# Kernel optimization log

Measured on AMD Instinct MI355X. Metric: run time of the kernel, lower is better.

## Reference

```python
import jax, jax.numpy as jnp
import numpy as np

B, N, D = 4, 2048, 1024
HEAD_DIMS = 128
NUM_HEADS = 8
PROJ = HEAD_DIMS * NUM_HEADS  # 1024


def setup_inputs() -> dict:
    key = jax.random.key(0)
    ks = jax.random.split(key, 5)
    # Weights stored as (in, out); xavier-normal-like scale
    def xavier(k, fan_in, fan_out):
        std = (2.0 / (fan_in + fan_out)) ** 0.5
        return jax.random.normal(k, (fan_in, fan_out), dtype=jnp.float32) * std
    return {
        "x": jax.random.normal(ks[0], (B, N, D), dtype=jnp.float32),
        "Wq": xavier(ks[1], D, PROJ),
        "Wk": xavier(ks[2], D, PROJ),
        "Wv": xavier(ks[3], D, PROJ),
        "Wo": xavier(ks[4], PROJ, PROJ),
    }


def reference(x, Wq, Wk, Wv, Wo):
    b, n, d = x.shape
    # QKV projections, split into heads: (b, h, n, hd)
    def split_heads(z):
        return z.reshape(b, n, NUM_HEADS, HEAD_DIMS).transpose(0, 2, 1, 3)
    q = split_heads(x @ Wq)
    k = split_heads(x @ Wk)
    v = split_heads(x @ Wv)
    scale = 1.0 / jnp.sqrt(jnp.float32(HEAD_DIMS))
    logits = jnp.einsum("bhqd,bhkd->bhqk", q, k) * scale
    weights = jax.nn.softmax(logits, axis=-1)
    out = jnp.einsum("bhqk,bhkd->bhqd", weights, v)
    out = out.transpose(0, 2, 1, 3).reshape(b, n, PROJ)
    return out @ Wo
```

## Files before the change

### kernel.cpp

```cpp
#include <hip/hip_runtime.h>
#include <hip/hip_bf16.h>


typedef __attribute__((ext_vector_type(8))) short short8;
typedef __attribute__((ext_vector_type(4))) short short4v;
typedef __attribute__((ext_vector_type(4))) float floatx4;

#define MFMA_BF16(a, b, c) __builtin_amdgcn_mfma_f32_16x16x32_bf16((a), (b), (c), 0, 0, 0)

static constexpr int BATCH  = 4;
static constexpr int NHEADS = 8;
static constexpr int SEQ    = 2048;
static constexpr int HD     = 128;
static constexpr int DMODEL = 1024;
static constexpr int MROWS  = BATCH * SEQ;
static constexpr int NQKV   = 3 * DMODEL;

static __device__ __forceinline__ short bf16bits(float v) {
    __hip_bfloat16 h = __float2bfloat16(v);
    return *reinterpret_cast<short*>(&h);
}

template <typename T>
static __device__ __forceinline__ short8 load8_bf16(const T* p) {
    if constexpr (sizeof(T) == 2) {
        return *(const short8*)p;
    } else {
        const float4 f0 = *(const float4*)p;
        const float4 f1 = *(const float4*)(p + 4);
        short8 r;
        r[0] = bf16bits(f0.x); r[1] = bf16bits(f0.y);
        r[2] = bf16bits(f0.z); r[3] = bf16bits(f0.w);
        r[4] = bf16bits(f1.x); r[5] = bf16bits(f1.y);
        r[6] = bf16bits(f1.z); r[7] = bf16bits(f1.w);
        return r;
    }
}

static __device__ __forceinline__ void storeC(float* C, size_t idx, float v) {
    C[idx] = v;
}
static __device__ __forceinline__ void storeC(__hip_bfloat16* C, size_t idx, float v) {
    C[idx] = __float2bfloat16(v);
}

static __device__ __forceinline__ void gload16(const short* g, short* l) {
    __builtin_amdgcn_global_load_lds(
        (const __attribute__((address_space(1))) void*)g,
        (__attribute__((address_space(3))) void*)l, 16, 0, 0);
}

__global__ __launch_bounds__(256)
void convert_bf16(const float* __restrict__ in, short* __restrict__ out)
{
    const size_t i = ((size_t)blockIdx.x * 256 + threadIdx.x) * 8;
    *(short8*)&out[i] = load8_bf16(&in[i]);
}

__global__ __launch_bounds__(256)
void transpose_w(const float* __restrict__ W, short* __restrict__ Wt, int K, int N)
{
    __shared__ short T[32][33];
    const int n0 = blockIdx.x * 32, k0 = blockIdx.y * 32;
    const int r = threadIdx.x >> 3, c4 = (threadIdx.x & 7) * 4;

    const float4 v = *(const float4*)&W[(size_t)(k0 + r) * N + n0 + c4];
    T[r][c4 + 0] = bf16bits(v.x);
    T[r][c4 + 1] = bf16bits(v.y);
    T[r][c4 + 2] = bf16bits(v.z);
    T[r][c4 + 3] = bf16bits(v.w);
    __syncthreads();

    short4v o;
    o[0] = T[c4 + 0][r]; o[1] = T[c4 + 1][r];
    o[2] = T[c4 + 2][r]; o[3] = T[c4 + 3][r];
    *(short4v*)&Wt[(size_t)(n0 + r) * K + k0 + c4] = o;
}

template <typename OutT, bool QKV>
__global__ __launch_bounds__(256)
void gemm128(const short* __restrict__ A, const short* __restrict__ Bt,
             OutT* __restrict__ C, int M, int N, int K)
{
    __shared__ __align__(16) short As[128 * 32];
    __shared__ __align__(16) short Bs[128 * 32];

    const int tid  = threadIdx.x;
    const int lane = tid & 63;
    const int w    = tid >> 6;
    const int quad = lane >> 4;
    const int l16  = lane & 15;

    const int m0 = blockIdx.x * 128;
    const int n0 = blockIdx.y * 128;
    const int wm = (w >> 1) * 64;
    const int wn = (w & 1) * 64;

    floatx4 acc[4][4] = {};

    const int srow = w * 32 + (lane >> 2);
    const int sk   = (lane & 3) ^ ((srow >> 1) & 3);
    const short* aG = A  + (size_t)(m0 + srow) * K + sk * 8;
    const short* bG = Bt + (size_t)(n0 + srow) * K + sk * 8;
    short* aL = As + w * 1024 + lane * 8;
    short* bL = Bs + w * 1024 + lane * 8;

    const int fsw = (l16 >> 1) & 3;

    for (int k0 = 0; k0 < K; k0 += 32) {
        __syncthreads();
        gload16(aG + k0,                   aL);
        gload16(aG + k0 + (size_t)16 * K,  aL + 512);
        gload16(bG + k0,                   bL);
        gload16(bG + k0 + (size_t)16 * K,  bL + 512);
        __syncthreads();

        short8 af[4], bf[4];
        #pragma unroll
        for (int mi = 0; mi < 4; ++mi)
            af[mi] = *(short8*)&As[(wm + mi * 16 + l16) * 32 + (quad ^ fsw) * 8];
        #pragma unroll
        for (int ni = 0; ni < 4; ++ni)
            bf[ni] = *(short8*)&Bs[(wn + ni * 16 + l16) * 32 + (quad ^ fsw) * 8];

        #pragma unroll
        for (int mi = 0; mi < 4; ++mi)
            #pragma unroll
            for (int ni = 0; ni < 4; ++ni)
                acc[mi][ni] = MFMA_BF16(af[mi], bf[ni], acc[mi][ni]);
    }

    const size_t bufElems = (size_t)MROWS * DMODEL;
    #pragma unroll
    for (int mi = 0; mi < 4; ++mi)
        #pragma unroll
        for (int ni = 0; ni < 4; ++ni)
            #pragma unroll
            for (int r = 0; r < 4; ++r) {
                const int m = m0 + wm + mi * 16 + quad * 4 + r;
                const int n = n0 + wn + ni * 16 + l16;
                const float v = acc[mi][ni][r];
                if constexpr (QKV) {
                    const int qkv = n >> 10, rem = n & 1023;
                    const int h = rem >> 7, d = rem & 127;
                    const int b = m >> 11, s = m & 2047;
                    if (qkv == 2)
                        storeC(C, 2 * bufElems +
                                  (((size_t)b * NHEADS + h) * HD + d) * SEQ + s, v);
                    else
                        storeC(C, qkv * bufElems +
                                  (((size_t)b * NHEADS + h) * SEQ + s) * HD + d, v);
                } else {
                    storeC(C, (size_t)m * N + n, v);
                }
            }
}

__global__ __launch_bounds__(256)
void attn_flash2(const short* __restrict__ Q, const short* __restrict__ K,
                 const short* __restrict__ Vt, __hip_bfloat16* __restrict__ O)
{
    __shared__ __align__(16) short Ks[32 * 128];
    __shared__ __align__(16) short Vs[128 * 32];
    __shared__ __align__(16) short Plds[4][16 * 40];

    const int tid  = threadIdx.x;
    const int lane = tid & 63;
    const int w    = tid >> 6;
    const int quad = lane >> 4;
    const int l16  = lane & 15;

    const int q0 = blockIdx.x * 64;
    const int h  = blockIdx.y;
    const int b  = blockIdx.z;

    const short* Qh  = Q  + (((size_t)b * NHEADS + h) * SEQ) * HD;
    const short* Kh  = K  + (((size_t)b * NHEADS + h) * SEQ) * HD;
    const short* Vth = Vt + (((size_t)b * NHEADS + h) * HD) * SEQ;

    const float scale = 0.08838834764831845f;

    const int qrow = q0 + w * 16 + l16;
    short8 qf[4];
    #pragma unroll
    for (int c = 0; c < 4; ++c)
        qf[c] = *(const short8*)&Qh[(size_t)qrow * HD + c * 32 + quad * 8];

    const int krow0 = w * 8 + (lane >> 4);
    const int kp    = lane & 15;
    const short* kG0 = Kh + (size_t)krow0 * HD + (kp ^ (krow0 & 15)) * 8;
    const short* kG1 = Kh + (size_t)(krow0 + 4) * HD + (kp ^ ((krow0 + 4) & 15)) * 8;
    short* kL0 = Ks + w * 1024 + lane * 8;
    short* kL1 = kL0 + 512;
    const int vrow0 = w * 32 + (lane >> 2);
    const int vp    = lane & 3;
    const short* vG0 = Vth + (size_t)vrow0 * SEQ + (vp ^ ((vrow0 >> 1) & 3)) * 8;
    const short* vG1 = vG0 + (size_t)16 * SEQ;
    short* vL0 = Vs + w * 1024 + lane * 8;
    short* vL1 = vL0 + 512;

    float lrow[4] = {0.f, 0.f, 0.f, 0.f};
    floatx4 acc[8] = {};

    const int fswK = l16;
    const int fswV = (l16 >> 1) & 3;
    short* Pw = &Plds[w][0];

    for (int kt = 0; kt < SEQ; kt += 32) {
        __syncthreads();
        gload16(kG0, kL0);
        gload16(kG1, kL1);
        gload16(vG0, vL0);
        gload16(vG1, vL1);
        kG0 += 32 * HD; kG1 += 32 * HD;
        vG0 += 32;      vG1 += 32;
        __syncthreads();

        floatx4 s0 = {}, s1 = {};
        #pragma unroll
        for (int c = 0; c < 4; ++c) {
            const int k_ = c * 4 + quad;
            short8 kf0 = *(short8*)&Ks[l16 * 128 + (k_ ^ fswK) * 8];
            short8 kf1 = *(short8*)&Ks[(16 + l16) * 128 + (k_ ^ fswK) * 8];
            s0 = MFMA_BF16(qf[c], kf0, s0);
            s1 = MFMA_BF16(qf[c], kf1, s1);
        }

        float p0[4], p1[4];
        #pragma unroll
        for (int r = 0; r < 4; ++r) {
            p0[r] = __expf(fminf(s0[r] * scale, 20.f));
            p1[r] = __expf(fminf(s1[r] * scale, 20.f));
            lrow[r] += p0[r] + p1[r];
        }

        #pragma unroll
        for (int r = 0; r < 4; ++r) {
            Pw[(quad * 4 + r) * 40 + l16]      = bf16bits(p0[r]);
            Pw[(quad * 4 + r) * 40 + 16 + l16] = bf16bits(p1[r]);
        }
        short8 pf = *(short8*)&Pw[l16 * 40 + quad * 8];

        #pragma unroll
        for (int hc = 0; hc < 8; ++hc) {
            short8 vf = *(short8*)&Vs[(hc * 16 + l16) * 32 + (quad ^ fswV) * 8];
            acc[hc] = MFMA_BF16(pf, vf, acc[hc]);
        }
    }

    #pragma unroll
    for (int r = 0; r < 4; ++r) {
        lrow[r] += __shfl_xor(lrow[r], 1);
        lrow[r] += __shfl_xor(lrow[r], 2);
        lrow[r] += __shfl_xor(lrow[r], 4);
        lrow[r] += __shfl_xor(lrow[r], 8);
    }

    #pragma unroll
    for (int hc = 0; hc < 8; ++hc)
        #pragma unroll
        for (int r = 0; r < 4; ++r) {
            const int row = q0 + w * 16 + quad * 4 + r;
            const float val = acc[hc][r] / fmaxf(lrow[r], 1e-30f);
            O[((size_t)b * SEQ + row) * DMODEL + h * HD + hc * 16 + l16] =
                __float2bfloat16(val);
        }
}

template <typename AT, typename OutT>
__global__ __launch_bounds__(256)
void gemm64(const AT* __restrict__ A, const float* __restrict__ W,
            OutT* __restrict__ C, int M, int N, int K, int headsplit)
{
    __shared__ __align__(16) short As[64][32];
    __shared__ __align__(16) short Bs[64][32];

    const int tid  = threadIdx.x;
    const int lane = tid & 63;
    const int w    = tid >> 6;
    const int quad = lane >> 4;
    const int l16  = lane & 15;

    const int m0 = blockIdx.x * 64;
    const int n0 = blockIdx.y * 64;
    const int wm = (w >> 1) * 32;
    const int wn = (w & 1) * 32;

    floatx4 acc[2][2] = {};

    const int arow = tid >> 2, acol = (tid & 3) * 8;
    const int brow = tid >> 3, bcol = (tid & 7) * 8;

    const AT*    aptr = A + (size_t)(m0 + arow) * K + acol;
    const float* bptr = W + (size_t)brow * N + n0 + bcol;

    for (int k0 = 0; k0 < K; k0 += 32) {
        short8 av = load8_bf16(aptr + k0);
        short8 bv = load8_bf16(bptr + (size_t)k0 * N);
        __syncthreads();
        *(short8*)&As[arow][acol] = av;
        #pragma unroll
        for (int j = 0; j < 8; ++j)
            Bs[bcol + j][brow] = bv[j];
        __syncthreads();

        short8 af0 = *(short8*)&As[wm + l16][quad * 8];
        short8 af1 = *(short8*)&As[wm + 16 + l16][quad * 8];
        short8 bf0 = *(short8*)&Bs[wn + l16][quad * 8];
        short8 bf1 = *(short8*)&Bs[wn + 16 + l16][quad * 8];

        acc[0][0] = MFMA_BF16(af0, bf0, acc[0][0]);
        acc[0][1] = MFMA_BF16(af0, bf1, acc[0][1]);
        acc[1][0] = MFMA_BF16(af1, bf0, acc[1][0]);
        acc[1][1] = MFMA_BF16(af1, bf1, acc[1][1]);
    }

    #pragma unroll
    for (int mi = 0; mi < 2; ++mi)
        #pragma unroll
        for (int ni = 0; ni < 2; ++ni)
            #pragma unroll
            for (int r = 0; r < 4; ++r) {
                const int m = m0 + wm + mi * 16 + quad * 4 + r;
                const int n = n0 + wn + ni * 16 + l16;
                const float v = acc[mi][ni][r];
                if (headsplit) {
                    const int b = m >> 11, nn = m & 2047;
                    const int h = n >> 7,  d  = n & 127;
                    storeC(C, (((size_t)b * NHEADS + h) * SEQ + nn) * HD + d, v);
                } else {
                    storeC(C, (size_t)m * N + n, v);
                }
            }
}

__global__ __launch_bounds__(256)
void attn_flash(const short* __restrict__ Q, const short* __restrict__ K,
                const short* __restrict__ V, __hip_bfloat16* __restrict__ O)
{
    __shared__ __align__(16) short Ks[32][136];
    __shared__ __align__(16) short Vtl[HD][40];
    __shared__ __align__(16) short Plds[4][16][40];

    const int tid  = threadIdx.x;
    const int lane = tid & 63;
    const int w    = tid >> 6;
    const int quad = lane >> 4;
    const int l16  = lane & 15;

    const int q0 = blockIdx.x * 64;
    const int h  = blockIdx.y;
    const int b  = blockIdx.z;

    const size_t headoff = ((size_t)b * NHEADS + h) * SEQ * HD;
    const short* Qh = Q + headoff;
    const short* Kh = K + headoff;
    const short* Vh = V + headoff;

    const float scale = 0.08838834764831845f;

    const int qrow = q0 + w * 16 + l16;
    short8 qf[4];
    #pragma unroll
    for (int c = 0; c < 4; ++c)
        qf[c] = *(const short8*)&Qh[(size_t)qrow * HD + c * 32 + quad * 8];

    float mrow[4], lrow[4];
    #pragma unroll
    for (int r = 0; r < 4; ++r) { mrow[r] = -1e30f; lrow[r] = 0.f; }
    floatx4 acc[8] = {};

    const int krow = tid >> 4, kcol = (tid & 15) * 8;
    const int vkey = tid & 31;
    const int vhd  = (tid >> 5) * 16;

    for (int kt = 0; kt < SEQ; kt += 32) {
        const short* Kt = Kh + (size_t)kt * HD;
        short8 k0v = *(const short8*)(Kt + (size_t)tid * 8);
        short8 k1v = *(const short8*)(Kt + (size_t)(tid + 256) * 8);
        short8 v0 = *(const short8*)&Vh[(size_t)(kt + vkey) * HD + vhd];
        short8 v1 = *(const short8*)&Vh[(size_t)(kt + vkey) * HD + vhd + 8];

        __syncthreads();
        *(short8*)&Ks[krow][kcol]      = k0v;
        *(short8*)&Ks[krow + 16][kcol] = k1v;
        #pragma unroll
        for (int j = 0; j < 8; ++j) {
            Vtl[vhd + j][vkey]     = v0[j];
            Vtl[vhd + 8 + j][vkey] = v1[j];
        }
        __syncthreads();

        floatx4 s0 = {}, s1 = {};
        #pragma unroll
        for (int c = 0; c < 4; ++c) {
            short8 kf0 = *(short8*)&Ks[l16][c * 32 + quad * 8];
            short8 kf1 = *(short8*)&Ks[16 + l16][c * 32 + quad * 8];
            s0 = MFMA_BF16(qf[c], kf0, s0);
            s1 = MFMA_BF16(qf[c], kf1, s1);
        }

        float p0[4], p1[4], alpha[4];
        #pragma unroll
        for (int r = 0; r < 4; ++r) {
            const float a  = s0[r] * scale;
            const float bb = s1[r] * scale;
            float mx = fmaxf(a, bb);
            mx = fmaxf(mx, __shfl_xor(mx, 1));
            mx = fmaxf(mx, __shfl_xor(mx, 2));
            mx = fmaxf(mx, __shfl_xor(mx, 4));
            mx = fmaxf(mx, __shfl_xor(mx, 8));
            const float mnew = fmaxf(mrow[r], mx);
            alpha[r] = __expf(mrow[r] - mnew);
            mrow[r]  = mnew;
            p0[r] = __expf(a - mnew);
            p1[r] = __expf(bb - mnew);
            float rs = p0[r] + p1[r];
            rs += __shfl_xor(rs, 1);
            rs += __shfl_xor(rs, 2);
            rs += __shfl_xor(rs, 4);
            rs += __shfl_xor(rs, 8);
            lrow[r] = lrow[r] * alpha[r] + rs;
        }
        #pragma unroll
        for (int hc = 0; hc < 8; ++hc)
            #pragma unroll
            for (int r = 0; r < 4; ++r)
                acc[hc][r] *= alpha[r];

        #pragma unroll
        for (int r = 0; r < 4; ++r) {
            Plds[w][quad * 4 + r][l16]      = bf16bits(p0[r]);
            Plds[w][quad * 4 + r][16 + l16] = bf16bits(p1[r]);
        }
        __syncthreads();

        short8 pf = *(short8*)&Plds[w][l16][quad * 8];
        #pragma unroll
        for (int hc = 0; hc < 8; ++hc) {
            short8 vf = *(short8*)&Vtl[hc * 16 + l16][quad * 8];
            acc[hc] = MFMA_BF16(pf, vf, acc[hc]);
        }
    }

    #pragma unroll
    for (int hc = 0; hc < 8; ++hc)
        #pragma unroll
        for (int r = 0; r < 4; ++r) {
            const int row = q0 + w * 16 + quad * 4 + r;
            const float val = acc[hc][r] / fmaxf(lrow[r], 1e-30f);
            O[((size_t)b * SEQ + row) * DMODEL + h * HD + hc * 16 + l16] =
                __float2bfloat16(val);
        }
}

extern "C" void kernel_launch(void* const* d_in, const int* in_sizes, int n_in,
                              void* d_out, int out_size, void* d_ws, size_t ws_size,
                              hipStream_t stream)
{
    const float* x  = (const float*)d_in[0];
    const float* Wq = (const float*)d_in[1];
    const float* Wk = (const float*)d_in[2];
    const float* Wv = (const float*)d_in[3];
    const float* Wo = (const float*)d_in[4];
    float* out = (float*)d_out;

    const size_t bufElems = (size_t)MROWS * DMODEL;
    const size_t MiB = 1024 * 1024;
    dim3 tt(256);

    if (ws_size >= 72 * MiB) {
        short* xb    = (short*)d_ws;
        short* Qb    = xb + bufElems;
        short* Kb    = Qb + bufElems;
        short* VtG   = Qb + 2 * bufElems;
        short* Wtqkv = xb + 4 * bufElems;
        short* Wto   = Wtqkv + 3 * (size_t)DMODEL * DMODEL;
        short* Ab    = xb;

        convert_bf16<<<dim3(MROWS * DMODEL / (256 * 8)), tt, 0, stream>>>(x, xb);

        dim3 tg(DMODEL / 32, DMODEL / 32);
        transpose_w<<<tg, tt, 0, stream>>>(Wq, Wtqkv,                               DMODEL, DMODEL);
        transpose_w<<<tg, tt, 0, stream>>>(Wk, Wtqkv + (size_t)DMODEL * DMODEL,     DMODEL, DMODEL);
        transpose_w<<<tg, tt, 0, stream>>>(Wv, Wtqkv + 2 * (size_t)DMODEL * DMODEL, DMODEL, DMODEL);
        transpose_w<<<tg, tt, 0, stream>>>(Wo, Wto,                                 DMODEL, DMODEL);

        gemm128<__hip_bfloat16, true><<<dim3(MROWS / 128, NQKV / 128), tt, 0, stream>>>(
            xb, Wtqkv, (__hip_bfloat16*)Qb, MROWS, NQKV, DMODEL);

        attn_flash2<<<dim3(SEQ / 64, NHEADS, BATCH), tt, 0, stream>>>(
            Qb, Kb, VtG, (__hip_bfloat16*)Ab);

        gemm128<float, false><<<dim3(MROWS / 128, DMODEL / 128), tt, 0, stream>>>(
            Ab, Wto, out, MROWS, DMODEL, DMODEL);
    } else {
        __hip_bfloat16* Qb = (__hip_bfloat16*)d_ws;
        __hip_bfloat16* Kb = Qb + bufElems;
        __hip_bfloat16* Vb = Kb + bufElems;
        __hip_bfloat16* Ab = Vb + bufElems;

        dim3 gg(MROWS / 64, DMODEL / 64);
        gemm64<float, __hip_bfloat16><<<gg, tt, 0, stream>>>(x, Wq, Qb, MROWS, DMODEL, DMODEL, 1);
        gemm64<float, __hip_bfloat16><<<gg, tt, 0, stream>>>(x, Wk, Kb, MROWS, DMODEL, DMODEL, 1);
        gemm64<float, __hip_bfloat16><<<gg, tt, 0, stream>>>(x, Wv, Vb, MROWS, DMODEL, DMODEL, 1);

        attn_flash<<<dim3(SEQ / 64, NHEADS, BATCH), tt, 0, stream>>>(
            (const short*)Qb, (const short*)Kb, (const short*)Vb, Ab);

        gemm64<short, float><<<gg, tt, 0, stream>>>(
            (const short*)Ab, Wo, out, MROWS, DMODEL, DMODEL, 0);
    }
}
```

Before: 318.9 us.

## Write V head-major and transpose separately; use 512-thread attention blocks

The QKV GEMM now writes V in the same head-major layout as Q and K, which avoids strided scattered stores in its epilogue. A separate transpose kernel then builds V^T through shared memory. The attention kernel goes to 512 threads (8 waves, 128 query rows per block), so each K/V tile loaded into LDS is shared by twice as many queries, and the head index is placed innermost in the grid. The softmax exponent uses exp2 with a pre-scaled constant. The cost is an extra kernel launch and an extra pass over V through memory.

```diff
diff --git a/kernel.cpp b/kernel.cpp
--- a/kernel.cpp
+++ b/kernel.cpp
@@ -77,6 +77,33 @@
     *(short4v*)&Wt[(size_t)(n0 + r) * K + k0 + c4] = o;
 }
 
+__global__ __launch_bounds__(256)
+void transpose_v(const short* __restrict__ V, short* __restrict__ Vt)
+{
+    __shared__ short T[64][72];
+    const int s0 = blockIdx.x * 64;
+    const int d0 = blockIdx.y * 64;
+    const int bh = blockIdx.z;
+    const short* Vi = V  + (size_t)bh * SEQ * HD;
+    short*       Vo = Vt + (size_t)bh * HD * SEQ;
+
+    const int r = threadIdx.x >> 3;
+    const int c = threadIdx.x & 7;
+
+    *(short8*)&T[r][c * 8]      = *(const short8*)&Vi[(size_t)(s0 + r) * HD + d0 + c * 8];
+    *(short8*)&T[r + 32][c * 8] = *(const short8*)&Vi[(size_t)(s0 + r + 32) * HD + d0 + c * 8];
+    __syncthreads();
+
+    short8 o0, o1;
+    #pragma unroll
+    for (int j = 0; j < 8; ++j) {
+        o0[j] = T[c * 8 + j][r];
+        o1[j] = T[c * 8 + j][r + 32];
+    }
+    *(short8*)&Vo[(size_t)(d0 + r) * SEQ + s0 + c * 8]      = o0;
+    *(short8*)&Vo[(size_t)(d0 + r + 32) * SEQ + s0 + c * 8] = o1;
+}
+
 template <typename OutT, bool QKV>
 __global__ __launch_bounds__(256)
 void gemm128(const short* __restrict__ A, const short* __restrict__ Bt,
@@ -144,25 +171,21 @@
                     const int qkv = n >> 10, rem = n & 1023;
                     const int h = rem >> 7, d = rem & 127;
                     const int b = m >> 11, s = m & 2047;
-                    if (qkv == 2)
-                        storeC(C, 2 * bufElems +
-                                  (((size_t)b * NHEADS + h) * HD + d) * SEQ + s, v);
-                    else
-                        storeC(C, qkv * bufElems +
-                                  (((size_t)b * NHEADS + h) * SEQ + s) * HD + d, v);
+                    storeC(C, qkv * bufElems +
+                              (((size_t)b * NHEADS + h) * SEQ + s) * HD + d, v);
                 } else {
                     storeC(C, (size_t)m * N + n, v);
                 }
             }
 }
 
-__global__ __launch_bounds__(256)
-void attn_flash2(const short* __restrict__ Q, const short* __restrict__ K,
+__global__ __launch_bounds__(512)
+void attn_flash3(const short* __restrict__ Q, const short* __restrict__ K,
                  const short* __restrict__ Vt, __hip_bfloat16* __restrict__ O)
 {
     __shared__ __align__(16) short Ks[32 * 128];
     __shared__ __align__(16) short Vs[128 * 32];
-    __shared__ __align__(16) short Plds[4][16 * 40];
+    __shared__ __align__(16) short Plds[8][16 * 40];
 
     const int tid  = threadIdx.x;
     const int lane = tid & 63;
@@ -170,15 +193,16 @@
     const int quad = lane >> 4;
     const int l16  = lane & 15;
 
-    const int q0 = blockIdx.x * 64;
-    const int h  = blockIdx.y;
-    const int b  = blockIdx.z;
+    const int h  = blockIdx.x & 7;
+    const int qi = blockIdx.x >> 3;
+    const int b  = blockIdx.y;
+    const int q0 = qi * 128;
 
     const short* Qh  = Q  + (((size_t)b * NHEADS + h) * SEQ) * HD;
     const short* Kh  = K  + (((size_t)b * NHEADS + h) * SEQ) * HD;
     const short* Vth = Vt + (((size_t)b * NHEADS + h) * HD) * SEQ;
 
-    const float scale = 0.08838834764831845f;
+    const float scale2 = 0.12752283786512624f;
 
     const int qrow = q0 + w * 16 + l16;
     short8 qf[4];
@@ -186,18 +210,12 @@
     for (int c = 0; c < 4; ++c)
         qf[c] = *(const short8*)&Qh[(size_t)qrow * HD + c * 32 + quad * 8];
 
-    const int krow0 = w * 8 + (lane >> 4);
-    const int kp    = lane & 15;
-    const short* kG0 = Kh + (size_t)krow0 * HD + (kp ^ (krow0 & 15)) * 8;
-    const short* kG1 = Kh + (size_t)(krow0 + 4) * HD + (kp ^ ((krow0 + 4) & 15)) * 8;
-    short* kL0 = Ks + w * 1024 + lane * 8;
-    short* kL1 = kL0 + 512;
-    const int vrow0 = w * 32 + (lane >> 2);
-    const int vp    = lane & 3;
-    const short* vG0 = Vth + (size_t)vrow0 * SEQ + (vp ^ ((vrow0 >> 1) & 3)) * 8;
-    const short* vG1 = vG0 + (size_t)16 * SEQ;
-    short* vL0 = Vs + w * 1024 + lane * 8;
-    short* vL1 = vL0 + 512;
+    const int krow = tid >> 4, kp = tid & 15;
+    const short* kG = Kh + (size_t)krow * HD + (kp ^ (krow & 15)) * 8;
+    short* kL = Ks + tid * 8;
+    const int vrow = tid >> 2, vp = tid & 3;
+    const short* vG = Vth + (size_t)vrow * SEQ + (vp ^ ((vrow >> 1) & 3)) * 8;
+    short* vL = Vs + tid * 8;
 
     float lrow[4] = {0.f, 0.f, 0.f, 0.f};
     floatx4 acc[8] = {};
@@ -208,12 +226,10 @@
 
     for (int kt = 0; kt < SEQ; kt += 32) {
         __syncthreads();
-        gload16(kG0, kL0);
-        gload16(kG1, kL1);
-        gload16(vG0, vL0);
-        gload16(vG1, vL1);
-        kG0 += 32 * HD; kG1 += 32 * HD;
-        vG0 += 32;      vG1 += 32;
+        gload16(kG, kL);
+        gload16(vG, vL);
+        kG += 32 * HD;
+        vG += 32;
         __syncthreads();
 
         floatx4 s0 = {}, s1 = {};
@@ -229,8 +245,8 @@
         float p0[4], p1[4];
         #pragma unroll
         for (int r = 0; r < 4; ++r) {
-            p0[r] = __expf(fminf(s0[r] * scale, 20.f));
-            p1[r] = __expf(fminf(s1[r] * scale, 20.f));
+            p0[r] = exp2f(fminf(s0[r] * scale2, 28.853901f));
+            p1[r] = exp2f(fminf(s1[r] * scale2, 28.853901f));
             lrow[r] += p0[r] + p1[r];
         }
 
@@ -472,11 +488,12 @@
     if (ws_size >= 72 * MiB) {
         short* xb    = (short*)d_ws;
         short* Qb    = xb + bufElems;
-        short* Kb    = Qb + bufElems;
-        short* VtG   = Qb + 2 * bufElems;
+        short* Kb    = xb + 2 * bufElems;
+        short* Vn    = xb + 3 * bufElems;
         short* Wtqkv = xb + 4 * bufElems;
         short* Wto   = Wtqkv + 3 * (size_t)DMODEL * DMODEL;
-        short* Ab    = xb;
+        short* VtG   = xb;
+        short* Ab    = Vn;
 
         convert_bf16<<<dim3(MROWS * DMODEL / (256 * 8)), tt, 0, stream>>>(x, xb);
 
@@ -489,7 +506,9 @@
         gemm128<__hip_bfloat16, true><<<dim3(MROWS / 128, NQKV / 128), tt, 0, stream>>>(
             xb, Wtqkv, (__hip_bfloat16*)Qb, MROWS, NQKV, DMODEL);
 
-        attn_flash2<<<dim3(SEQ / 64, NHEADS, BATCH), tt, 0, stream>>>(
+        transpose_v<<<dim3(SEQ / 64, HD / 64, BATCH * NHEADS), tt, 0, stream>>>(Vn, VtG);
+
+        attn_flash3<<<dim3(NHEADS * (SEQ / 128), BATCH), dim3(512), 0, stream>>>(
             Qb, Kb, VtG, (__hip_bfloat16*)Ab);
 
         gemm128<float, false><<<dim3(MROWS / 128, DMODEL / 128), tt, 0, stream>>>(
```

New measurement: 308.9 us. 3.1% less time.
